# Kernel optimization log

Hardware: AMD Instinct MI355X
Metric: run time of the kernel (lower is better)

Reference implementation:

```python
import jax, jax.numpy as jnp
import numpy as np

B, S, D = 4, 2048, 1024
H, HD = 16, 64
ROT_DIM = 64
ROT_BASE = 10000.0


def setup_inputs() -> dict:
    key = jax.random.key(0)
    ks = jax.random.split(key, 5)
    return {
        "hidden_states": jax.random.normal(ks[0], (B, S, D), dtype=jnp.float32),
        "Wqkv_w": jax.random.normal(ks[1], (3 * D, D), dtype=jnp.float32) * 0.02,
        "Wqkv_b": jax.random.normal(ks[2], (3 * D,), dtype=jnp.float32) * 0.02,
        "Wo_w": jax.random.normal(ks[3], (D, D), dtype=jnp.float32) * 0.02,
        "Wo_b": jax.random.normal(ks[4], (D,), dtype=jnp.float32) * 0.02,
    }


def _rope_cos_sin(seqlen, dtype):
    inv_freq = 1.0 / (ROT_BASE ** (jnp.arange(0, ROT_DIM, 2, dtype=jnp.float32) / ROT_DIM))
    t = jnp.arange(seqlen, dtype=jnp.float32)
    freqs = jnp.einsum("s,f->sf", t, inv_freq)  # (S, ROT_DIM//2)
    return jnp.cos(freqs).astype(dtype), jnp.sin(freqs).astype(dtype)


def _apply_rope(x, cos, sin):
    # x: (B, S, H, HD), non-interleaved rotary on first ROT_DIM dims
    ro, pas = x[..., :ROT_DIM], x[..., ROT_DIM:]
    x1, x2 = ro[..., : ROT_DIM // 2], ro[..., ROT_DIM // 2 :]
    c = cos[None, :, None, :]  # (1, S, 1, ROT_DIM//2)
    s = sin[None, :, None, :]
    rot = jnp.concatenate([x1 * c - x2 * s, x1 * s + x2 * c], axis=-1)
    return jnp.concatenate([rot, pas], axis=-1) if pas.shape[-1] else rot


def reference(hidden_states, Wqkv_w, Wqkv_b, Wo_w, Wo_b):
    b, s, d = hidden_states.shape
    qkv = hidden_states @ Wqkv_w.T + Wqkv_b  # (B, S, 3D)
    qkv = qkv.reshape(b, s, 3, H, HD)
    q, k, v = qkv[:, :, 0], qkv[:, :, 1], qkv[:, :, 2]  # each (B, S, H, HD)
    cos, sin = _rope_cos_sin(s, hidden_states.dtype)
    q = _apply_rope(q, cos, sin)
    k = _apply_rope(k, cos, sin)
    scale = 1.0 / jnp.sqrt(jnp.asarray(HD, hidden_states.dtype))
    scores = jnp.einsum("bqhd,bkhd->bhqk", q, k) * scale
    probs = jax.nn.softmax(scores, axis=-1)
    attn = jnp.einsum("bhqk,bkhd->bqhd", probs, v)  # (B, S, H, HD)
    attn = attn.reshape(b, s, d)
    return attn @ Wo_w.T + Wo_b
```

## Files before the change

### kernel.cpp

```cpp
#include <hip/hip_runtime.h>
#include <hip/hip_bf16.h>
#include <cstdint>
#include <cstddef>

typedef __bf16 bf16;
typedef __bf16 bf16x4 __attribute__((ext_vector_type(4)));
typedef __bf16 bf16x8 __attribute__((ext_vector_type(8)));
typedef float f32x4 __attribute__((ext_vector_type(4)));

#define NB 4
#define NS 2048
#define ND 1024
#define NH 16
#define NHD 64
#define NM (NB * NS)

#define QSCALE 0.18033688011112042f

__device__ inline void lds_dma16(const bf16* g, bf16* l) {
    __builtin_amdgcn_global_load_lds(
        (const __attribute__((address_space(1))) void*)g,
        (__attribute__((address_space(3))) void*)l, 16, 0, 0);
}

#define NHS4 2097152
#define NWQ4 786432
#define NWO4 262144
__global__ void prep_kernel(const float4* __restrict__ hs, const float4* __restrict__ wq,
                            const float4* __restrict__ wo,
                            float* __restrict__ cost, float* __restrict__ sint,
                            bf16x4* __restrict__ X, bf16x4* __restrict__ Wb,
                            bf16x4* __restrict__ Wob) {
    int i = blockIdx.x * 256 + threadIdx.x;
    if (i < NS * 32) {
        int s = i >> 5, f = i & 31;
        float inv = exp2f(-(float)f * (13.287712379549449f / 32.0f));
        float ang = (float)s * inv;
        cost[i] = cosf(ang);
        sint[i] = sinf(ang);
    }
    if (i < NHS4) {
        float4 v = hs[i];
        bf16x4 r = {(bf16)v.x, (bf16)v.y, (bf16)v.z, (bf16)v.w};
        X[i] = r;
    } else if (i < NHS4 + NWQ4) {
        int j = i - NHS4;
        float4 v = wq[j];
        bf16x4 r = {(bf16)v.x, (bf16)v.y, (bf16)v.z, (bf16)v.w};
        Wb[j] = r;
    } else {
        int j = i - NHS4 - NWQ4;
        float4 v = wo[j];
        bf16x4 r = {(bf16)v.x, (bf16)v.y, (bf16)v.z, (bf16)v.w};
        Wob[j] = r;
    }
}

__global__ void cvt_bf16_kernel(const float4* __restrict__ in, bf16x4* __restrict__ out) {
    int i = blockIdx.x * 256 + threadIdx.x;
    float4 v = in[i];
    bf16x4 r = {(bf16)v.x, (bf16)v.y, (bf16)v.z, (bf16)v.w};
    out[i] = r;
}

__global__ void __launch_bounds__(256) qkv_rope_gemm(
    const bf16* __restrict__ A, const bf16* __restrict__ W,
    const float* __restrict__ bias,
    const float* __restrict__ cost, const float* __restrict__ sint,
    bf16* __restrict__ Qw, bf16* __restrict__ Kw, bf16* __restrict__ Vt) {
    __shared__ __attribute__((aligned(16))) bf16 lA[128 * 64];
    __shared__ __attribute__((aligned(16))) bf16 lB[128 * 64];

    int t = threadIdx.x, lane = t & 63, w = t >> 6;
    int col = lane & 15, quad = lane >> 4;
    int m0 = blockIdx.y * 128, n0 = blockIdx.x * 128;
    int wm = (w >> 1) * 64, wn = (w & 1) * 64;

    f32x4 acc[4][4];
#pragma unroll
    for (int i = 0; i < 4; ++i)
#pragma unroll
        for (int j = 0; j < 4; ++j) acc[i][j] = (f32x4){0.f, 0.f, 0.f, 0.f};

    int srow = t >> 3;
    int sslot = (t & 7) ^ (srow & 7);
    const bf16* gA = A + (size_t)(m0 + srow) * ND + sslot * 8;
    const bf16* gB = W + (size_t)(n0 + srow) * ND + sslot * 8;

    int aRow = (wm + col) * 64;
    int bRow = (wn + col) * 64;

    for (int kt = 0; kt < 16; ++kt) {
        int kc = kt * 64;
#pragma unroll
        for (int c = 0; c < 4; ++c) {
            lds_dma16(gA + (size_t)(c * 32) * ND + kc, &lA[c * 2048 + t * 8]);
            lds_dma16(gB + (size_t)(c * 32) * ND + kc, &lB[c * 2048 + t * 8]);
        }
        __syncthreads();
#pragma unroll
        for (int kh = 0; kh < 2; ++kh) {
            int sk = ((kh * 4 + quad) ^ (col & 7)) * 8;
            bf16x8 af[4], bg[4];
#pragma unroll
            for (int i = 0; i < 4; ++i)
                af[i] = *(const bf16x8*)&lA[aRow + i * 1024 + sk];
#pragma unroll
            for (int j = 0; j < 4; ++j)
                bg[j] = *(const bf16x8*)&lB[bRow + j * 1024 + sk];
#pragma unroll
            for (int i = 0; i < 4; ++i)
#pragma unroll
                for (int j = 0; j < 4; ++j)
                    acc[i][j] = __builtin_amdgcn_mfma_f32_16x16x32_bf16(af[i], bg[j], acc[i][j], 0, 0, 0);
        }
        __syncthreads();
    }

    int nseg = n0 + wn;
    int which = nseg >> 10;
    int h = (nseg >> 6) & (NH - 1);
    float bj[4];
#pragma unroll
    for (int j = 0; j < 4; ++j) bj[j] = bias[nseg + j * 16 + col];

    if (which == 2) {
        int mbase = m0 + wm;
        int b = mbase >> 11;
        bf16* dsth = Vt + (size_t)(b * NH + h) * NHD * NS;
#pragma unroll
        for (int i = 0; i < 4; ++i) {
            int s = ((mbase + i * 16) & (NS - 1)) + quad * 4;
#pragma unroll
            for (int j = 0; j < 4; ++j) {
                bf16x4 pv = {(bf16)(acc[i][j][0] + bj[j]), (bf16)(acc[i][j][1] + bj[j]),
                             (bf16)(acc[i][j][2] + bj[j]), (bf16)(acc[i][j][3] + bj[j])};
                *(bf16x4*)(dsth + (size_t)(j * 16 + col) * NS + s) = pv;
            }
        }
    } else {
        float sc = which ? 1.0f : QSCALE;
#pragma unroll
        for (int i = 0; i < 4; ++i) {
#pragma unroll
            for (int r = 0; r < 4; ++r) {
                int m = m0 + wm + i * 16 + quad * 4 + r;
                int b = m >> 11, s = m & (NS - 1);
                float v0 = acc[i][0][r] + bj[0];
                float v1 = acc[i][1][r] + bj[1];
                float v2 = acc[i][2][r] + bj[2];
                float v3 = acc[i][3][r] + bj[3];
                bf16* dst = (which ? Kw : Qw) + ((size_t)(b * NH + h) * NS + s) * NHD;
                float c0 = cost[s * 32 + col], s0 = sint[s * 32 + col];
                float c1 = cost[s * 32 + 16 + col], s1 = sint[s * 32 + 16 + col];
                dst[col] = (bf16)((v0 * c0 - v2 * s0) * sc);
                dst[16 + col] = (bf16)((v1 * c1 - v3 * s1) * sc);
                dst[32 + col] = (bf16)((v0 * s0 + v2 * c0) * sc);
                dst[48 + col] = (bf16)((v1 * s1 + v3 * c1) * sc);
            }
        }
    }
}

__global__ void __launch_bounds__(256, 2) attn_kernel(
    const bf16* __restrict__ Qw, const bf16* __restrict__ Kw,
    const bf16* __restrict__ Vt, bf16* __restrict__ X) {
    const int LDK = 72;
    const int LV = 36;
    __shared__ __attribute__((aligned(16))) bf16 lK[2][32 * LDK];
    __shared__ __attribute__((aligned(16))) bf16 lV[2][64 * LV];

    int t = threadIdx.x, lane = t & 63, w = t >> 6;
    int col = lane & 15, q = lane >> 4;
    int bh = blockIdx.y, b = bh >> 4, h = bh & 15;
    int q0 = blockIdx.x * 256 + w * 64;
    const bf16* Qh = Qw + (size_t)bh * NS * NHD;
    const bf16* Kh = Kw + (size_t)bh * NS * NHD;
    const bf16* Vh = Vt + (size_t)bh * NHD * NS;

    int krow = t >> 3, kc = t & 7;
    int vrow = t >> 2, vc = t & 3;
    const bf16* gK = Kh + (size_t)krow * NHD + kc * 8;
    const bf16* gV = Vh + (size_t)vrow * NS + vc * 8;
    int wKoff = krow * LDK + kc * 8;
    int wVoff = vrow * LV + vc * 8;

    bf16x8 bQ[4][2];
#pragma unroll
    for (int mb = 0; mb < 4; ++mb)
#pragma unroll
        for (int h2 = 0; h2 < 2; ++h2)
            bQ[mb][h2] = *(const bf16x8*)(Qh + (size_t)(q0 + mb * 16 + col) * NHD + h2 * 32 + q * 8);

    f32x4 o[4][4];
#pragma unroll
    for (int mb = 0; mb < 4; ++mb)
#pragma unroll
        for (int hb = 0; hb < 4; ++hb) o[mb][hb] = (f32x4){0.f, 0.f, 0.f, 0.f};
    f32x4 dacc[4];
#pragma unroll
    for (int mb = 0; mb < 4; ++mb) dacc[mb] = (f32x4){0.f, 0.f, 0.f, 0.f};

    const bf16 one = (bf16)1.0f;
    bf16x8 ones = {one, one, one, one, one, one, one, one};

    bf16x8 kr[2], vr[2];
    kr[0] = *(const bf16x8*)gK;
    vr[0] = *(const bf16x8*)gV;
    kr[1] = *(const bf16x8*)(gK + (size_t)32 * NHD);
    vr[1] = *(const bf16x8*)(gV + 32);
    *(bf16x8*)&lK[0][wKoff] = kr[0];
    *(bf16x8*)&lV[0][wVoff] = vr[0];

#pragma unroll 2
    for (int it = 0; it < 64; ++it) {
        __syncthreads();
        int cur = it & 1, nxt = cur ^ 1;
        if (it + 2 < 64) {
            kr[cur] = *(const bf16x8*)(gK + (size_t)(it + 2) * 32 * NHD);
            vr[cur] = *(const bf16x8*)(gV + (it + 2) * 32);
        }

        bf16x8 aK[2][2];
#pragma unroll
        for (int tb = 0; tb < 2; ++tb)
#pragma unroll
            for (int h2 = 0; h2 < 2; ++h2)
                aK[tb][h2] = *(const bf16x8*)&lK[cur][(tb * 16 + col) * LDK + h2 * 32 + q * 8];
        bf16x8 vf[4];
#pragma unroll
        for (int hb = 0; hb < 4; ++hb) {
            const bf16* vp = &lV[cur][(hb * 16 + col) * LV + q * 4];
            bf16x4 lo = *(const bf16x4*)vp;
            bf16x4 hi = *(const bf16x4*)(vp + 16);
            vf[hb] = __builtin_shufflevector(lo, hi, 0, 1, 2, 3, 4, 5, 6, 7);
        }
        __builtin_amdgcn_s_setprio(1);
#pragma unroll
        for (int mb = 0; mb < 4; ++mb) {
            f32x4 s0 = (f32x4){0.f, 0.f, 0.f, 0.f};
            f32x4 s1 = (f32x4){0.f, 0.f, 0.f, 0.f};
            s0 = __builtin_amdgcn_mfma_f32_16x16x32_bf16(aK[0][0], bQ[mb][0], s0, 0, 0, 0);
            s0 = __builtin_amdgcn_mfma_f32_16x16x32_bf16(aK[0][1], bQ[mb][1], s0, 0, 0, 0);
            s1 = __builtin_amdgcn_mfma_f32_16x16x32_bf16(aK[1][0], bQ[mb][0], s1, 0, 0, 0);
            s1 = __builtin_amdgcn_mfma_f32_16x16x32_bf16(aK[1][1], bQ[mb][1], s1, 0, 0, 0);
            bf16x8 pf;
#pragma unroll
            for (int r = 0; r < 4; ++r) {
                float p0 = __builtin_amdgcn_exp2f(s0[r]);
                float p1 = __builtin_amdgcn_exp2f(s1[r]);
                pf[r] = (bf16)p0;
                pf[4 + r] = (bf16)p1;
            }
            dacc[mb] = __builtin_amdgcn_mfma_f32_16x16x32_bf16(ones, pf, dacc[mb], 0, 0, 0);
#pragma unroll
            for (int hb = 0; hb < 4; ++hb)
                o[mb][hb] = __builtin_amdgcn_mfma_f32_16x16x32_bf16(vf[hb], pf, o[mb][hb], 0, 0, 0);
        }
        __builtin_amdgcn_s_setprio(0);

        if (it + 1 < 64) {
            *(bf16x8*)&lK[nxt][wKoff] = kr[nxt];
            *(bf16x8*)&lV[nxt][wVoff] = vr[nxt];
        }
    }

#pragma unroll
    for (int mb = 0; mb < 4; ++mb) {
        float linv = 1.0f / dacc[mb][0];
        int s = q0 + mb * 16 + col;
        bf16* dst = X + (size_t)(b * NS + s) * ND + h * NHD;
#pragma unroll
        for (int hb = 0; hb < 4; ++hb) {
            bf16x4 ov = {(bf16)(o[mb][hb][0] * linv), (bf16)(o[mb][hb][1] * linv),
                         (bf16)(o[mb][hb][2] * linv), (bf16)(o[mb][hb][3] * linv)};
            *(bf16x4*)(dst + hb * 16 + q * 4) = ov;
        }
    }
}

__global__ void __launch_bounds__(256) out_gemm(
    const bf16* __restrict__ A, const bf16* __restrict__ W,
    const float* __restrict__ bias, float* __restrict__ out) {
    __shared__ __attribute__((aligned(16))) bf16 lA[128 * 64];
    __shared__ __attribute__((aligned(16))) bf16 lB[128 * 64];

    int t = threadIdx.x, lane = t & 63, w = t >> 6;
    int col = lane & 15, quad = lane >> 4;
    int m0 = blockIdx.y * 128, n0 = blockIdx.x * 128;
    int wm = (w >> 1) * 64, wn = (w & 1) * 64;

    f32x4 acc[4][4];
#pragma unroll
    for (int i = 0; i < 4; ++i)
#pragma unroll
        for (int j = 0; j < 4; ++j) acc[i][j] = (f32x4){0.f, 0.f, 0.f, 0.f};

    int srow = t >> 3;
    int sslot = (t & 7) ^ (srow & 7);
    const bf16* gA = A + (size_t)(m0 + srow) * ND + sslot * 8;
    const bf16* gB = W + (size_t)(n0 + srow) * ND + sslot * 8;
    int aRow = (wm + col) * 64;
    int bRow = (wn + col) * 64;

    for (int kt = 0; kt < 16; ++kt) {
        int kc = kt * 64;
#pragma unroll
        for (int c = 0; c < 4; ++c) {
            lds_dma16(gA + (size_t)(c * 32) * ND + kc, &lA[c * 2048 + t * 8]);
            lds_dma16(gB + (size_t)(c * 32) * ND + kc, &lB[c * 2048 + t * 8]);
        }
        __syncthreads();
#pragma unroll
        for (int kh = 0; kh < 2; ++kh) {
            int sk = ((kh * 4 + quad) ^ (col & 7)) * 8;
            bf16x8 af[4], bg[4];
#pragma unroll
            for (int i = 0; i < 4; ++i)
                af[i] = *(const bf16x8*)&lA[aRow + i * 1024 + sk];
#pragma unroll
            for (int j = 0; j < 4; ++j)
                bg[j] = *(const bf16x8*)&lB[bRow + j * 1024 + sk];
#pragma unroll
            for (int i = 0; i < 4; ++i)
#pragma unroll
                for (int j = 0; j < 4; ++j)
                    acc[i][j] = __builtin_amdgcn_mfma_f32_16x16x32_bf16(af[i], bg[j], acc[i][j], 0, 0, 0);
        }
        __syncthreads();
    }

    float bj[4];
#pragma unroll
    for (int j = 0; j < 4; ++j) bj[j] = bias[n0 + wn + j * 16 + col];
#pragma unroll
    for (int i = 0; i < 4; ++i)
#pragma unroll
        for (int r = 0; r < 4; ++r) {
            int m = m0 + wm + i * 16 + quad * 4 + r;
#pragma unroll
            for (int j = 0; j < 4; ++j)
                out[(size_t)m * ND + n0 + wn + j * 16 + col] = acc[i][j][r] + bj[j];
        }
}

extern "C" void kernel_launch(void* const* d_in, const int* in_sizes, int n_in,
                              void* d_out, int out_size, void* d_ws, size_t ws_size,
                              hipStream_t stream) {
    const float* hs = (const float*)d_in[0];
    const float* Wqkv = (const float*)d_in[1];
    const float* bqkv = (const float*)d_in[2];
    const float* Wo = (const float*)d_in[3];
    const float* bo = (const float*)d_in[4];
    float* out = (float*)d_out;

    char* ws = (char*)d_ws;
    float* cost = (float*)ws;
    float* sint = cost + NS * 32;
    bf16* Qw = (bf16*)(ws + 524288);
    bf16* Kw = Qw + (size_t)NB * NH * NS * NHD;
    bf16* Vt = Kw + (size_t)NB * NH * NS * NHD;
    bf16* X = Vt + (size_t)NB * NH * NS * NHD;
    bf16* Wqkv_b = (bf16*)d_out;

    const size_t base_end = 524288 + (size_t)4 * NB * NH * NS * NHD * 2;
    bool fuse_wo = ws_size >= base_end + (size_t)ND * ND * 2;
    bf16* Wo_b = fuse_wo ? (bf16*)(ws + base_end) : Qw;

    int prep_blocks = (NHS4 + NWQ4 + (fuse_wo ? NWO4 : 0)) / 256;
    prep_kernel<<<dim3(prep_blocks), dim3(256), 0, stream>>>(
        (const float4*)hs, (const float4*)Wqkv, (const float4*)Wo,
        cost, sint, (bf16x4*)X, (bf16x4*)Wqkv_b, (bf16x4*)Wo_b);
    qkv_rope_gemm<<<dim3(3 * ND / 128, NM / 128), dim3(256), 0, stream>>>(
        X, Wqkv_b, bqkv, cost, sint, Qw, Kw, Vt);
    attn_kernel<<<dim3(NS / 256, NB * NH), dim3(256), 0, stream>>>(Qw, Kw, Vt, X);
    if (!fuse_wo)
        cvt_bf16_kernel<<<dim3(ND * ND / 4 / 256), dim3(256), 0, stream>>>(
            (const float4*)Wo, (bf16x4*)Wo_b);
    out_gemm<<<dim3(ND / 128, NM / 128), dim3(256), 0, stream>>>(X, Wo_b, bo, out);
}
```

Before: 256.9 us.

## Split attention key range across two warp groups with LDS reduction

The attention block grows from 256 to 512 threads. The second group of four warps processes the other half of each 64-key tile, for the same queries as the first group. Partial outputs and row sums are combined through shared memory at the end. This doubles the waves per workgroup and halves the serial key-loop iterations, which should hide latency better. The cost is an extra LDS reduction with syncs per query block and higher LDS use per block.

```diff
diff --git a/kernel.cpp b/kernel.cpp
--- a/kernel.cpp
+++ b/kernel.cpp
@@ -162,28 +162,32 @@
     }
 }
 
-__global__ void __launch_bounds__(256, 2) attn_kernel(
+__global__ void __launch_bounds__(512, 4) attn_kernel(
     const bf16* __restrict__ Qw, const bf16* __restrict__ Kw,
     const bf16* __restrict__ Vt, bf16* __restrict__ X) {
     const int LDK = 72;
-    const int LV = 36;
-    __shared__ __attribute__((aligned(16))) bf16 lK[2][32 * LDK];
-    __shared__ __attribute__((aligned(16))) bf16 lV[2][64 * LV];
+    const int LV = 68;
+    const int KSZ = 64 * LDK;
+    const int VSZ = 64 * LV;
+    __shared__ __attribute__((aligned(16))) bf16 smem[2 * KSZ + 2 * VSZ];
+    bf16* lKb = smem;
+    bf16* lVb = smem + 2 * KSZ;
+    float* rsc = (float*)(smem + 2 * KSZ);
 
     int t = threadIdx.x, lane = t & 63, w = t >> 6;
     int col = lane & 15, q = lane >> 4;
     int bh = blockIdx.y, b = bh >> 4, h = bh & 15;
-    int q0 = blockIdx.x * 256 + w * 64;
+    int ks = (w >> 2) * 32;
+    int q0 = blockIdx.x * 256 + (w & 3) * 64;
     const bf16* Qh = Qw + (size_t)bh * NS * NHD;
     const bf16* Kh = Kw + (size_t)bh * NS * NHD;
     const bf16* Vh = Vt + (size_t)bh * NHD * NS;
 
-    int krow = t >> 3, kc = t & 7;
-    int vrow = t >> 2, vc = t & 3;
-    const bf16* gK = Kh + (size_t)krow * NHD + kc * 8;
-    const bf16* gV = Vh + (size_t)vrow * NS + vc * 8;
-    int wKoff = krow * LDK + kc * 8;
-    int wVoff = vrow * LV + vc * 8;
+    int srow = t >> 3, scol = (t & 7) * 8;
+    const bf16* gK = Kh + (size_t)srow * NHD + scol;
+    const bf16* gV = Vh + (size_t)srow * NS + scol;
+    int wKoff = srow * LDK + scol;
+    int wVoff = srow * LV + scol;
 
     bf16x8 bQ[4][2];
 #pragma unroll
@@ -207,30 +211,32 @@
     bf16x8 kr[2], vr[2];
     kr[0] = *(const bf16x8*)gK;
     vr[0] = *(const bf16x8*)gV;
-    kr[1] = *(const bf16x8*)(gK + (size_t)32 * NHD);
-    vr[1] = *(const bf16x8*)(gV + 32);
-    *(bf16x8*)&lK[0][wKoff] = kr[0];
-    *(bf16x8*)&lV[0][wVoff] = vr[0];
+    kr[1] = *(const bf16x8*)(gK + (size_t)64 * NHD);
+    vr[1] = *(const bf16x8*)(gV + 64);
+    *(bf16x8*)&lKb[wKoff] = kr[0];
+    *(bf16x8*)&lVb[wVoff] = vr[0];
 
 #pragma unroll 2
-    for (int it = 0; it < 64; ++it) {
+    for (int it = 0; it < 32; ++it) {
         __syncthreads();
         int cur = it & 1, nxt = cur ^ 1;
-        if (it + 2 < 64) {
-            kr[cur] = *(const bf16x8*)(gK + (size_t)(it + 2) * 32 * NHD);
-            vr[cur] = *(const bf16x8*)(gV + (it + 2) * 32);
-        }
-
+        if (it + 2 < 32) {
+            kr[cur] = *(const bf16x8*)(gK + (size_t)(it + 2) * 64 * NHD);
+            vr[cur] = *(const bf16x8*)(gV + (it + 2) * 64);
+        }
+
+        const bf16* lKc = lKb + cur * KSZ;
+        const bf16* lVc = lVb + cur * VSZ;
         bf16x8 aK[2][2];
 #pragma unroll
         for (int tb = 0; tb < 2; ++tb)
 #pragma unroll
             for (int h2 = 0; h2 < 2; ++h2)
-                aK[tb][h2] = *(const bf16x8*)&lK[cur][(tb * 16 + col) * LDK + h2 * 32 + q * 8];
+                aK[tb][h2] = *(const bf16x8*)&lKc[(ks + tb * 16 + col) * LDK + h2 * 32 + q * 8];
         bf16x8 vf[4];
 #pragma unroll
         for (int hb = 0; hb < 4; ++hb) {
-            const bf16* vp = &lV[cur][(hb * 16 + col) * LV + q * 4];
+            const bf16* vp = &lVc[(hb * 16 + col) * LV + ks + q * 4];
             bf16x4 lo = *(const bf16x4*)vp;
             bf16x4 hi = *(const bf16x4*)(vp + 16);
             vf[hb] = __builtin_shufflevector(lo, hi, 0, 1, 2, 3, 4, 5, 6, 7);
@@ -259,22 +265,36 @@
         }
         __builtin_amdgcn_s_setprio(0);
 
-        if (it + 1 < 64) {
-            *(bf16x8*)&lK[nxt][wKoff] = kr[nxt];
-            *(bf16x8*)&lV[nxt][wVoff] = vr[nxt];
+        if (it + 1 < 32) {
+            *(bf16x8*)&lKb[nxt * KSZ + wKoff] = kr[nxt];
+            *(bf16x8*)&lVb[nxt * VSZ + wVoff] = vr[nxt];
         }
     }
 
 #pragma unroll
     for (int mb = 0; mb < 4; ++mb) {
-        float linv = 1.0f / dacc[mb][0];
-        int s = q0 + mb * 16 + col;
-        bf16* dst = X + (size_t)(b * NS + s) * ND + h * NHD;
-#pragma unroll
-        for (int hb = 0; hb < 4; ++hb) {
-            bf16x4 ov = {(bf16)(o[mb][hb][0] * linv), (bf16)(o[mb][hb][1] * linv),
-                         (bf16)(o[mb][hb][2] * linv), (bf16)(o[mb][hb][3] * linv)};
-            *(bf16x4*)(dst + hb * 16 + q * 4) = ov;
+        __syncthreads();
+        float* sc = rsc + ((w & 3) * 64 + lane) * 17;
+        if (w >= 4) {
+#pragma unroll
+            for (int hb = 0; hb < 4; ++hb)
+#pragma unroll
+                for (int r = 0; r < 4; ++r) sc[hb * 4 + r] = o[mb][hb][r];
+            sc[16] = dacc[mb][0];
+        }
+        __syncthreads();
+        if (w < 4) {
+            float linv = 1.0f / (dacc[mb][0] + sc[16]);
+            int s = q0 + mb * 16 + col;
+            bf16* dst = X + (size_t)(b * NS + s) * ND + h * NHD;
+#pragma unroll
+            for (int hb = 0; hb < 4; ++hb) {
+                bf16x4 ov = {(bf16)((o[mb][hb][0] + sc[hb * 4 + 0]) * linv),
+                             (bf16)((o[mb][hb][1] + sc[hb * 4 + 1]) * linv),
+                             (bf16)((o[mb][hb][2] + sc[hb * 4 + 2]) * linv),
+                             (bf16)((o[mb][hb][3] + sc[hb * 4 + 3]) * linv)};
+                *(bf16x4*)(dst + hb * 16 + q * 4) = ov;
+            }
         }
     }
 }
@@ -373,7 +393,7 @@
         cost, sint, (bf16x4*)X, (bf16x4*)Wqkv_b, (bf16x4*)Wo_b);
     qkv_rope_gemm<<<dim3(3 * ND / 128, NM / 128), dim3(256), 0, stream>>>(
         X, Wqkv_b, bqkv, cost, sint, Qw, Kw, Vt);
-    attn_kernel<<<dim3(NS / 256, NB * NH), dim3(256), 0, stream>>>(Qw, Kw, Vt, X);
+    attn_kernel<<<dim3(NS / 256, NB * NH), dim3(512), 0, stream>>>(Qw, Kw, Vt, X);
     if (!fuse_wo)
         cvt_bf16_kernel<<<dim3(ND * ND / 4 / 256), dim3(256), 0, stream>>>(
             (const float4*)Wo, (bf16x4*)Wo_b);
```

New measurement: 618.4 us. +140.7%, slower.
